# Optimization experiments

Hardware: AMD Instinct MI355X
Metric: run time of the kernel (lower is better)

Reference implementation:

```python
import jax, jax.numpy as jnp
import numpy as np

H = 8
D_MODEL = 1024
D_K = D_MODEL // H
NEG = -1000000000.0


def layer_norm(x, a, b, eps=1e-06):
    # torch std: unbiased (ddof=1); module divides by (std + eps)
    mean = jnp.mean(x, axis=-1, keepdims=True)
    var = jnp.sum((x - mean) ** 2, axis=-1, keepdims=True) / (x.shape[-1] - 1)
    std = jnp.sqrt(var)
    return a * (x - mean) / (std + eps) + b


def setup_inputs() -> dict:
    key = jax.random.key(0)
    ks = jax.random.split(key, 12)
    B, S, D = 8, 1024, D_MODEL
    inp = {
        "query": jax.random.normal(ks[0], (B, S, D), jnp.float32),
        "value": jax.random.normal(ks[1], (B, S, D), jnp.float32),
        "key": jax.random.normal(ks[2], (B, S, D), jnp.float32),
        "mask": jax.random.randint(ks[3], (B, S), 0, 2, jnp.int32),
        "ln_a": jnp.ones((D,), jnp.float32),
        "ln_b": jnp.zeros((D,), jnp.float32),
        "wq": jax.random.normal(ks[4], (D, D), jnp.float32) * 0.02,
        "bq": jnp.zeros((D,), jnp.float32),
        "wk": jax.random.normal(ks[5], (D, D), jnp.float32) * 0.02,
        "bk": jnp.zeros((D,), jnp.float32),
        "wv": jax.random.normal(ks[6], (D, D), jnp.float32) * 0.02,
        "bv": jnp.zeros((D,), jnp.float32),
        "w_aoa": jax.random.normal(ks[7], (2 * D, 2 * D), jnp.float32) * 0.02,  # [out, in]
        "b_aoa": jnp.zeros((2 * D,), jnp.float32),
    }
    return inp


def reference(query, value, key, mask, ln_a, ln_b, wq, bq, wk, bk, wv, bv, w_aoa, b_aoa):
    B, S, D = query.shape
    # mask [B,S] -> [B,1,1,S]
    m = mask[:, None, None, :]
    # norm_q
    q = layer_norm(query, ln_a, ln_b)
    # QKV projections, split heads -> [B,H,S,Dk]
    def split_heads(x):
        return x.reshape(B, -1, H, D_K).transpose(0, 2, 1, 3)
    q_ = split_heads(q @ wq.T + bq)
    k_ = split_heads(key @ wk.T + bk)
    v_ = split_heads(value @ wv.T + bv)
    scores = jnp.einsum("bhqd,bhkd->bhqk", q_, k_) / jnp.sqrt(jnp.float32(D_K))
    scores = jnp.where(m == 0, NEG, scores)
    p = jax.nn.softmax(scores, axis=-1)
    x = jnp.einsum("bhqk,bhkd->bhqd", p, v_)
    x = x.transpose(0, 2, 1, 3).reshape(B, S, D)
    # AoA: concat with (normed) query, linear to 2D, GLU
    z = jnp.concatenate([x, q], axis=-1) @ w_aoa.T + b_aoa
    a, g = jnp.split(z, 2, axis=-1)
    return a * jax.nn.sigmoid(g)
```

## Files before the change

kernel.cpp:

```cpp
#include <hip/hip_runtime.h>

typedef __attribute__((ext_vector_type(8))) __bf16 bf16x8;
typedef __attribute__((ext_vector_type(4))) float f32x4;
typedef __attribute__((ext_vector_type(16))) float f32x16;
typedef __attribute__((ext_vector_type(2))) int i32x2;

__device__ __forceinline__ ushort f2b(float f) {
    uint u = __builtin_bit_cast(uint, f);
    u += 0x7fffu + ((u >> 16) & 1u);
    return (ushort)(u >> 16);
}
__device__ __forceinline__ float b2f(ushort h) {
    uint u = ((uint)h) << 16;
    return __builtin_bit_cast(float, u);
}
__device__ __forceinline__ uint cvtpk(float a, float b) {
    uint r;
    asm("v_cvt_pk_bf16_f32 %0, %1, %2" : "=v"(r) : "v"(a), "v"(b));
    return r;
}

__global__ __launch_bounds__(256) void cast2_kernel(const float* __restrict__ s0,
                                                    const float* __restrict__ s1,
                                                    ushort* __restrict__ dst) {
    int bid = blockIdx.x;
    const float* src = (bid < 8192) ? s0 : s1;
    size_t so = ((size_t)(bid & 8191) * 256 + threadIdx.x) * 4;
    float4 v = *(const float4*)(src + so);
    ushort4 o;
    o.x = f2b(v.x); o.y = f2b(v.y); o.z = f2b(v.z); o.w = f2b(v.w);
    *(ushort4*)(dst + (size_t)bid * 1024 + threadIdx.x * 4) = o;
}

__global__ __launch_bounds__(256) void cast3_kernel(const float* __restrict__ s0,
                                                    const float* __restrict__ s1,
                                                    const float* __restrict__ s2,
                                                    ushort* __restrict__ dst) {
    int bid = blockIdx.x;
    const float* src = (bid < 1024) ? s0 : ((bid < 2048) ? s1 : s2);
    size_t so = ((size_t)(bid & 1023) * 256 + threadIdx.x) * 4;
    float4 v = *(const float4*)(src + so);
    ushort4 o;
    o.x = f2b(v.x); o.y = f2b(v.y); o.z = f2b(v.z); o.w = f2b(v.w);
    *(ushort4*)(dst + (size_t)bid * 1024 + threadIdx.x * 4) = o;
}

__global__ __launch_bounds__(256) void cast_permute_aoa(const float* __restrict__ src,
                                                        ushort* __restrict__ dst) {
    int n1 = blockIdx.x >> 1;
    int c = (blockIdx.x & 1) * 1024 + threadIdx.x * 4;
    int q = ((n1 & 63) | ((n1 >> 7) << 6)) + ((n1 >> 6) & 1) * 1024;
    float4 v = *(const float4*)(src + (size_t)q * 2048 + c);
    ushort4 o;
    o.x = f2b(v.x); o.y = f2b(v.y); o.z = f2b(v.z); o.w = f2b(v.w);
    *(ushort4*)(dst + (size_t)n1 * 2048 + c) = o;
}

__global__ __launch_bounds__(256) void ln_kernel(const float* __restrict__ x,
                                                 const float* __restrict__ ga,
                                                 const float* __restrict__ be,
                                                 ushort* __restrict__ xq) {
    const int row = blockIdx.x, tid = threadIdx.x;
    __shared__ float red[4];
    float4 v = ((const float4*)(x + (size_t)row * 1024))[tid];
    float sm = v.x + v.y + v.z + v.w;
    for (int off = 32; off; off >>= 1) sm += __shfl_xor(sm, off);
    if ((tid & 63) == 0) red[tid >> 6] = sm;
    __syncthreads();
    float mean = (red[0] + red[1] + red[2] + red[3]) * (1.f / 1024.f);
    __syncthreads();
    float dx = v.x - mean, dy = v.y - mean, dz = v.z - mean, dw = v.w - mean;
    float s2 = dx * dx + dy * dy + dz * dz + dw * dw;
    for (int off = 32; off; off >>= 1) s2 += __shfl_xor(s2, off);
    if ((tid & 63) == 0) red[tid >> 6] = s2;
    __syncthreads();
    float var = (red[0] + red[1] + red[2] + red[3]) * (1.f / 1023.f);
    float inv = 1.f / (sqrtf(var) + 1e-6f);
    float4 g = ((const float4*)ga)[tid];
    float4 bb = ((const float4*)be)[tid];
    ushort4 o;
    o.x = f2b(g.x * dx * inv + bb.x);
    o.y = f2b(g.y * dy * inv + bb.y);
    o.z = f2b(g.z * dz * inv + bb.z);
    o.w = f2b(g.w * dw * inv + bb.w);
    *(ushort4*)&xq[(size_t)row * 2048 + 1024 + tid * 4] = o;
}

template <int MODE>
__global__ __launch_bounds__(512, 2) void gemm6(const ushort* __restrict__ Aq, int ldaq,
                                                const ushort* __restrict__ B, int ldb,
                                                const float* __restrict__ bias0,
                                                void* __restrict__ out0,
                                                int K, int NB) {
    __shared__ ushort lds[2][32768];

    const int tid = threadIdx.x;
    const int w = tid >> 6, l = tid & 63;
    const int wr = w >> 2, wcn = w & 3;
    const int r16 = l & 15, g4 = l >> 4;

    const int bid = blockIdx.x;
    const int cpx = gridDim.x >> 3;
    const int swz = (bid & 7) * cpx + (bid >> 3);
    const int m0 = (swz / NB) * 256;
    const int n0 = (swz % NB) * 256;

    const ushort* A = Aq;
    const int lda = ldaq;

    const int srow8 = l >> 3;
    const int sxor8 = ((l & 7) ^ srow8) * 8;
    const ushort* As0 = A + (size_t)(m0 + w * 8 + srow8) * lda + sxor8;
    const ushort* Bs0 = B + (size_t)(n0 + w * 8 + srow8) * ldb + sxor8;

    f32x4 acc[8][4];
#pragma unroll
    for (int i = 0; i < 8; i++)
#pragma unroll
        for (int j = 0; j < 4; j++) acc[i][j] = (f32x4){0.f, 0.f, 0.f, 0.f};

    const int sw16 = (r16 & 7) << 4;
    char* ldsb = (char*)&lds[0][0];

#define STAGE_H(sel_, HS_, kt_)                                                            \
    do {                                                                                   \
        const int mat_ = (HS_)&1, half_ = (HS_) >> 1;                                      \
        const ushort* sb_ = mat_ ? Bs0 : As0;                                              \
        const int ld_ = mat_ ? ldb : lda;                                                  \
        _Pragma("unroll") for (int li_ = 0; li_ < 2; li_++) {                              \
            const ushort* src_ = sb_ + (size_t)(half_ * 128 + li_ * 64) * ld_ + (kt_)*64;  \
            int dst_ = (sel_)*65536 + mat_ * 32768 + half_ * 16384 + li_ * 8192 + w * 1024;\
            __builtin_amdgcn_global_load_lds(                                              \
                (const __attribute__((address_space(1))) void*)src_,                       \
                (__attribute__((address_space(3))) void*)(ldsb + dst_), 16, 0, 0);         \
        }                                                                                  \
    } while (0)

    auto LDA4 = [&](bf16x8 (&dst)[4][2], int sel, int half) {
#pragma unroll
        for (int ai = 0; ai < 4; ai++)
#pragma unroll
            for (int ks = 0; ks < 2; ks++)
                dst[ai][ks] = *(const bf16x8*)(ldsb + sel * 65536 + half * 16384 +
                                               (wr * 16 + 32 * ai + r16) * 128 +
                                               ((ks * 64 + g4 * 16) ^ sw16));
    };
    auto LDB2 = [&](bf16x8 (&dst)[2][2], int sel, int half) {
#pragma unroll
        for (int bi = 0; bi < 2; bi++)
#pragma unroll
            for (int ks = 0; ks < 2; ks++)
                dst[bi][ks] = *(const bf16x8*)(ldsb + sel * 65536 + 32768 + half * 16384 +
                                               (wcn * 16 + 64 * bi + r16) * 128 +
                                               ((ks * 64 + g4 * 16) ^ sw16));
    };
    auto MM = [&](bf16x8 (&af)[4][2], bf16x8 (&bf)[2][2], int A0, int B0) {
        __builtin_amdgcn_s_setprio(1);
#pragma unroll
        for (int ks = 0; ks < 2; ks++)
#pragma unroll
            for (int ai = 0; ai < 4; ai++)
#pragma unroll
                for (int bi = 0; bi < 2; bi++)
                    acc[A0 + ai][B0 + bi] = __builtin_amdgcn_mfma_f32_16x16x32_bf16(
                        af[ai][ks], bf[bi][ks], acc[A0 + ai][B0 + bi], 0, 0, 0);
        __builtin_amdgcn_s_setprio(0);
    };

    const int NT = K >> 6;

    STAGE_H(0, 0, 0); STAGE_H(0, 1, 0); STAGE_H(0, 2, 0); STAGE_H(0, 3, 0);
    STAGE_H(1, 0, 1); STAGE_H(1, 1, 1); STAGE_H(1, 2, 1);
    asm volatile("s_waitcnt vmcnt(10)" ::: "memory");
    __builtin_amdgcn_s_barrier();

    bf16x8 aL[4][2], aH[4][2], bL[2][2], bH[2][2];

    for (int t = 0; t < NT - 2; ++t) {
        const int sel = t & 1;
        LDA4(aL, sel, 0); LDB2(bL, sel, 0);
        STAGE_H(sel ^ 1, 3, t + 1);
        __builtin_amdgcn_s_barrier();
        MM(aL, bL, 0, 0);
        asm volatile("s_waitcnt vmcnt(10)" ::: "memory");
        __builtin_amdgcn_s_barrier();
        LDA4(aH, sel, 1);
        STAGE_H(sel, 0, t + 2);
        __builtin_amdgcn_s_barrier();
        MM(aH, bL, 4, 0);
        asm volatile("s_waitcnt vmcnt(10)" ::: "memory");
        __builtin_amdgcn_s_barrier();
        LDB2(bH, sel, 1);
        STAGE_H(sel, 1, t + 2);
        __builtin_amdgcn_s_barrier();
        MM(aH, bH, 4, 2);
        __builtin_amdgcn_s_barrier();
        STAGE_H(sel, 2, t + 2);
        __builtin_amdgcn_s_barrier();
        MM(aL, bH, 0, 2);
        asm volatile("s_waitcnt vmcnt(10)" ::: "memory");
        __builtin_amdgcn_s_barrier();
    }
    {
        const int sel = (NT - 2) & 1;
        LDA4(aL, sel, 0); LDB2(bL, sel, 0);
        STAGE_H(sel ^ 1, 3, NT - 1);
        __builtin_amdgcn_s_barrier();
        MM(aL, bL, 0, 0);
        asm volatile("s_waitcnt vmcnt(10)" ::: "memory");
        __builtin_amdgcn_s_barrier();
        LDA4(aH, sel, 1);
        __builtin_amdgcn_s_barrier();
        MM(aH, bL, 4, 0);
        asm volatile("s_waitcnt vmcnt(8)" ::: "memory");
        __builtin_amdgcn_s_barrier();
        LDB2(bH, sel, 1);
        __builtin_amdgcn_s_barrier();
        MM(aH, bH, 4, 2);
        __builtin_amdgcn_s_barrier();
        MM(aL, bH, 0, 2);
        asm volatile("s_waitcnt vmcnt(4)" ::: "memory");
        __builtin_amdgcn_s_barrier();
    }
    {
        const int sel = (NT - 1) & 1;
        LDA4(aL, sel, 0); LDB2(bL, sel, 0);
        __builtin_amdgcn_s_barrier();
        MM(aL, bL, 0, 0);
        asm volatile("s_waitcnt vmcnt(2)" ::: "memory");
        __builtin_amdgcn_s_barrier();
        LDA4(aH, sel, 1);
        __builtin_amdgcn_s_barrier();
        MM(aH, bL, 4, 0);
        asm volatile("s_waitcnt vmcnt(0)" ::: "memory");
        __builtin_amdgcn_s_barrier();
        LDB2(bH, sel, 1);
        MM(aH, bH, 4, 2);
        MM(aL, bH, 0, 2);
    }
#undef STAGE_H

    float* out = (float*)out0;
#pragma unroll
    for (int bp = 0; bp < 2; bp++) {
        int j = (n0 >> 1) + wcn * 16 + 64 * bp + r16;
        float bsa = bias0[j];
        float bsg = bias0[j + 1024];
#pragma unroll
        for (int a_ = 0; a_ < 8; a_++) {
            int mr = m0 + wr * 16 + 32 * a_ + g4 * 4;
#pragma unroll
            for (int r = 0; r < 4; r++) {
                float av = acc[a_][2 * bp][r] + bsa;
                float gv = acc[a_][2 * bp + 1][r] + bsg;
                out[(size_t)(mr + r) * 1024 + j] = av * (1.f / (1.f + __expf(-gv)));
            }
        }
    }
}

__global__ __launch_bounds__(512, 2) void gemm7(const ushort* __restrict__ Aq, int ldaq,
                                                const ushort* __restrict__ Ak,
                                                const ushort* __restrict__ Av,
                                                const ushort* __restrict__ B, int ldb,
                                                const float* __restrict__ bias0,
                                                const float* __restrict__ bias1,
                                                const float* __restrict__ bias2,
                                                ushort* __restrict__ out0,
                                                ushort* __restrict__ out1,
                                                ushort* __restrict__ out2,
                                                float qscale) {
    __shared__ ushort lds[2][24576];

    const int tid = threadIdx.x;
    const int w = tid >> 6, l = tid & 63;
    const int wr = w >> 2, wcn = w & 3;
    const int r16 = l & 15, g4 = l >> 4;

    const int bid = blockIdx.x;
    const int cpx = gridDim.x >> 3;
    const int swz = (bid & 7) * cpx + (bid >> 3);
    const int m0 = (swz / 12) * 128;
    const int n0 = (swz % 12) * 256;

    const int region = n0 >> 10;
    const ushort* A = region == 0 ? Aq : (region == 1 ? Ak : Av);
    const int lda = region == 0 ? ldaq : 1024;

    const int srow8 = l >> 3;
    const int sxor8 = ((l & 7) ^ srow8) * 8;
    const ushort* As0 = A + (size_t)(m0 + w * 8 + srow8) * lda + sxor8;
    const ushort* Bs0 = B + (size_t)(n0 + w * 8 + srow8) * ldb + sxor8;

    f32x4 acc[4][4];
#pragma unroll
    for (int i = 0; i < 4; i++)
#pragma unroll
        for (int j = 0; j < 4; j++) acc[i][j] = (f32x4){0.f, 0.f, 0.f, 0.f};

    const int sw16 = (r16 & 7) << 4;
    char* ldsb = (char*)&lds[0][0];

#define STAGE_A(sel_, h_, kt_)                                                             \
    __builtin_amdgcn_global_load_lds(                                                      \
        (const __attribute__((address_space(1))) void*)(As0 + (size_t)((h_)*64) * lda + (kt_)*64), \
        (__attribute__((address_space(3))) void*)(ldsb + (sel_)*49152 + (h_)*8192 + w * 1024), 16, 0, 0)
#define STAGE_B(sel_, h_, li_, kt_)                                                        \
    __builtin_amdgcn_global_load_lds(                                                      \
        (const __attribute__((address_space(1))) void*)(Bs0 + (size_t)((h_)*128 + (li_)*64) * ldb + (kt_)*64), \
        (__attribute__((address_space(3))) void*)(ldsb + (sel_)*49152 + 16384 + (h_)*16384 + (li_)*8192 + w * 1024), 16, 0, 0)

    auto LDA2 = [&](bf16x8 (&dst)[2][2], int sel, int half) {
#pragma unroll
        for (int ai = 0; ai < 2; ai++)
#pragma unroll
            for (int ks = 0; ks < 2; ks++)
                dst[ai][ks] = *(const bf16x8*)(ldsb + sel * 49152 + half * 8192 +
                                               (wr * 16 + 32 * ai + r16) * 128 +
                                               ((ks * 64 + g4 * 16) ^ sw16));
    };
    auto LDB2 = [&](bf16x8 (&dst)[2][2], int sel, int half) {
#pragma unroll
        for (int bi = 0; bi < 2; bi++)
#pragma unroll
            for (int ks = 0; ks < 2; ks++)
                dst[bi][ks] = *(const bf16x8*)(ldsb + sel * 49152 + 16384 + half * 16384 +
                                               (wcn * 16 + 64 * bi + r16) * 128 +
                                               ((ks * 64 + g4 * 16) ^ sw16));
    };
    auto MM = [&](bf16x8 (&af)[2][2], bf16x8 (&bf)[2][2], int A0, int B0) {
        __builtin_amdgcn_s_setprio(1);
#pragma unroll
        for (int ks = 0; ks < 2; ks++)
#pragma unroll
            for (int ai = 0; ai < 2; ai++)
#pragma unroll
                for (int bi = 0; bi < 2; bi++)
                    acc[A0 + ai][B0 + bi] = __builtin_amdgcn_mfma_f32_16x16x32_bf16(
                        af[ai][ks], bf[bi][ks], acc[A0 + ai][B0 + bi], 0, 0, 0);
        __builtin_amdgcn_s_setprio(0);
    };

    const int NT = 16;

    STAGE_A(0, 0, 0); STAGE_B(0, 0, 0, 0); STAGE_B(0, 0, 1, 0);
    STAGE_A(0, 1, 0); STAGE_B(0, 1, 0, 0); STAGE_B(0, 1, 1, 0);
    STAGE_A(1, 0, 1); STAGE_B(1, 0, 0, 1); STAGE_B(1, 0, 1, 1);
    STAGE_A(1, 1, 1);
    asm volatile("s_waitcnt vmcnt(7)" ::: "memory");
    __builtin_amdgcn_s_barrier();

    bf16x8 aL[2][2], aH[2][2], bL[2][2], bH[2][2];

    for (int t = 0; t < NT - 2; ++t) {
        const int sel = t & 1;
        LDA2(aL, sel, 0); LDB2(bL, sel, 0);
        STAGE_B(sel ^ 1, 1, 0, t + 1); STAGE_B(sel ^ 1, 1, 1, t + 1);
        __builtin_amdgcn_s_barrier();
        MM(aL, bL, 0, 0);
        asm volatile("s_waitcnt vmcnt(8)" ::: "memory");
        __builtin_amdgcn_s_barrier();
        LDA2(aH, sel, 1);
        STAGE_A(sel, 0, t + 2);
        __builtin_amdgcn_s_barrier();
        MM(aH, bL, 2, 0);
        asm volatile("s_waitcnt vmcnt(7)" ::: "memory");
        __builtin_amdgcn_s_barrier();
        LDB2(bH, sel, 1);
        STAGE_B(sel, 0, 0, t + 2); STAGE_B(sel, 0, 1, t + 2);
        __builtin_amdgcn_s_barrier();
        MM(aH, bH, 2, 2);
        __builtin_amdgcn_s_barrier();
        STAGE_A(sel, 1, t + 2);
        __builtin_amdgcn_s_barrier();
        MM(aL, bH, 0, 2);
        asm volatile("s_waitcnt vmcnt(7)" ::: "memory");
        __builtin_amdgcn_s_barrier();
    }
    {
        const int sel = (NT - 2) & 1;
        LDA2(aL, sel, 0); LDB2(bL, sel, 0);
        STAGE_B(sel ^ 1, 1, 0, NT - 1); STAGE_B(sel ^ 1, 1, 1, NT - 1);
        __builtin_amdgcn_s_barrier();
        MM(aL, bL, 0, 0);
        asm volatile("s_waitcnt vmcnt(8)" ::: "memory");
        __builtin_amdgcn_s_barrier();
        LDA2(aH, sel, 1);
        __builtin_amdgcn_s_barrier();
        MM(aH, bL, 2, 0);
        asm volatile("s_waitcnt vmcnt(6)" ::: "memory");
        __builtin_amdgcn_s_barrier();
        LDB2(bH, sel, 1);
        __builtin_amdgcn_s_barrier();
        MM(aH, bH, 2, 2);
        __builtin_amdgcn_s_barrier();
        MM(aL, bH, 0, 2);
        asm volatile("s_waitcnt vmcnt(3)" ::: "memory");
        __builtin_amdgcn_s_barrier();
    }
    {
        const int sel = (NT - 1) & 1;
        LDA2(aL, sel, 0); LDB2(bL, sel, 0);
        __builtin_amdgcn_s_barrier();
        MM(aL, bL, 0, 0);
        asm volatile("s_waitcnt vmcnt(2)" ::: "memory");
        __builtin_amdgcn_s_barrier();
        LDA2(aH, sel, 1);
        __builtin_amdgcn_s_barrier();
        MM(aH, bL, 2, 0);
        asm volatile("s_waitcnt vmcnt(0)" ::: "memory");
        __builtin_amdgcn_s_barrier();
        LDB2(bH, sel, 1);
        MM(aH, bH, 2, 2);
        MM(aL, bH, 0, 2);
    }
#undef STAGE_A
#undef STAGE_B

    const int nr0 = n0 & 1023;
    const float* bias = region == 0 ? bias0 : (region == 1 ? bias1 : bias2);
    const float scale = region == 0 ? qscale : 1.f;
    if (region < 2) {
        ushort* C = region == 0 ? out0 : out1;
#pragma unroll
        for (int b_ = 0; b_ < 4; b_++) {
            int n = nr0 + wcn * 16 + 64 * b_ + r16;
            float bs = bias[n];
#pragma unroll
            for (int a_ = 0; a_ < 4; a_++) {
                int mr = m0 + wr * 16 + 32 * a_ + g4 * 4;
#pragma unroll
                for (int r = 0; r < 4; r++)
                    C[(size_t)(mr + r) * 1024 + n] = f2b((acc[a_][b_][r] + bs) * scale);
            }
        }
    } else {
        ushort* Vt = out2;
#pragma unroll
        for (int b_ = 0; b_ < 4; b_++) {
            int n = nr0 + wcn * 16 + 64 * b_ + r16;
            float bs = bias[n];
            int h = n >> 7, d = n & 127;
#pragma unroll
            for (int a_ = 0; a_ < 4; a_++) {
                int mr = m0 + wr * 16 + 32 * a_ + g4 * 4;
                int bb = mr >> 10, s_ = mr & 1023;
                ushort4 o;
                o.x = f2b(acc[a_][b_][0] + bs);
                o.y = f2b(acc[a_][b_][1] + bs);
                o.z = f2b(acc[a_][b_][2] + bs);
                o.w = f2b(acc[a_][b_][3] + bs);
                *(ushort4*)&Vt[((size_t)(bb * 8 + h) * 128 + d) * 1024 + s_] = o;
            }
        }
    }
}

__global__ __launch_bounds__(256, 2) void attn_kernel(const ushort* __restrict__ Q,
                                                      const ushort* __restrict__ Kt,
                                                      const ushort* __restrict__ Vt,
                                                      const int* __restrict__ mask,
                                                      ushort* __restrict__ xq) {
    __shared__ ushort Ks[2][8192];
    __shared__ ushort Vs[2][8192];

    const int tid = threadIdx.x;
    const int l = tid & 63, wid = tid >> 6;
    const int ql = l & 31, hi = l >> 5;
    const int id = blockIdx.x;
    const int bh = ((id >> 6) << 3) | (id & 7);
    const int qb = (id >> 3) & 7;
    const int b = bh >> 3, h = bh & 7;
    const int q0 = qb * 128 + wid * 32;

    bf16x8 qf[8];
    const ushort* Qrow = Q + (size_t)(b * 1024 + q0 + ql) * 1024 + h * 128 + hi * 8;
#pragma unroll
    for (int ks = 0; ks < 8; ks++) qf[ks] = *(const bf16x8*)(Qrow + ks * 16);

    const ushort* Kg = Kt + ((size_t)b * 1024) * 1024 + h * 128;
    const ushort* Vg = Vt + (size_t)(b * 8 + h) * 128 * 1024;
    const int* mptr = mask + b * 1024;

    f32x16 xacc[4];
#pragma unroll
    for (int i = 0; i < 4; i++)
#pragma unroll
        for (int r = 0; r < 16; r++) xacc[i][r] = 0.f;
    float mrow = -INFINITY, lrow = 0.f, sclp = 0.f;
    bf16x8 pa[4];

    auto STAGE_K = [&](int sel, int t) {
        const int kv0 = t * 64;
#pragma unroll
        for (int it = 0; it < 4; ++it) {
            int ob = it * 4096 + wid * 1024;
            int o = ob + l * 16;
            int row = o >> 8;
            int sc = (o & 255) ^ ((row & 7) << 4);
            const ushort* src = Kg + (size_t)(kv0 + row) * 1024 + (sc >> 1);
            __builtin_amdgcn_global_load_lds((const __attribute__((address_space(1))) void*)src,
                (__attribute__((address_space(3))) void*)((char*)&Ks[sel][0] + ob), 16, 0, 0);
        }
    };
    auto STAGE_V = [&](int sel, int t) {
        const int kv0 = t * 64;
#pragma unroll
        for (int it = 0; it < 4; ++it) {
            int ob = it * 4096 + wid * 1024;
            int o = ob + l * 16;
            int d = o >> 7;
            int sc = (o & 127) ^ ((d & 7) << 4);
            const ushort* src = Vg + (size_t)d * 1024 + kv0 + (sc >> 1);
            __builtin_amdgcn_global_load_lds((const __attribute__((address_space(1))) void*)src,
                (__attribute__((address_space(3))) void*)((char*)&Vs[sel][0] + ob), 16, 0, 0);
        }
    };

    auto QK = [&](f32x16 (&s)[2], int sel, unsigned long long wt) {
        const char* Kb_ = (const char*)&Ks[sel][0];
#pragma unroll
        for (int sub = 0; sub < 2; sub++) {
            f32x16 sacc;
#pragma unroll
            for (int r = 0; r < 16; r++) sacc[r] = 0.f;
            const int rowk = sub * 32 + ql;
            const char* kr = Kb_ + rowk * 256;
            const int sw = (rowk & 7) << 4;
            __builtin_amdgcn_s_setprio(1);
#pragma unroll
            for (int ks = 0; ks < 8; ks++) {
                bf16x8 kfr = *(const bf16x8*)(kr + ((ks * 32 + hi * 16) ^ sw));
                sacc = __builtin_amdgcn_mfma_f32_32x32x16_bf16(kfr, qf[ks], sacc, 0, 0, 0);
            }
            __builtin_amdgcn_s_setprio(0);
#pragma unroll
            for (int q2 = 0; q2 < 4; q2++) {
                uint nib = (uint)(wt >> (8 * q2 + 4 * hi + 32 * sub)) & 15u;
#pragma unroll
                for (int r = 0; r < 4; r++)
                    if (!((nib >> r) & 1u)) sacc[4 * q2 + r] = -1e9f;
            }
            s[sub] = sacc;
        }
    };
    auto PV = [&](int sel) {
        const char* Vb_ = (const char*)&Vs[sel][0];
#pragma unroll
        for (int df = 0; df < 4; df++)
#pragma unroll
            for (int r = 0; r < 16; r++) xacc[df][r] *= sclp;
        __builtin_amdgcn_s_setprio(1);
#pragma unroll
        for (int ks2 = 0; ks2 < 4; ks2++) {
#pragma unroll
            for (int df = 0; df < 4; df++) {
                const int d = df * 32 + ql;
                bf16x8 vfr = *(const bf16x8*)(Vb_ + d * 128 + ((ks2 * 32 + hi * 16) ^ ((d & 7) << 4)));
                xacc[df] = __builtin_amdgcn_mfma_f32_32x32x16_bf16(vfr, pa[ks2], xacc[df], 0, 0, 0);
            }
        }
        __builtin_amdgcn_s_setprio(0);
    };
    auto SOFTMAX = [&](f32x16 (&s)[2]) {
        float pmax = -INFINITY;
#pragma unroll
        for (int res = 0; res < 2; res++)
#pragma unroll
            for (int r = 0; r < 16; r++) pmax = fmaxf(pmax, s[res][r]);
        pmax = fmaxf(pmax, __shfl_xor(pmax, 32));
        float mn = fmaxf(mrow, pmax);
        sclp = __expf(mrow - mn);
        mrow = mn;
        float rsum = 0.f;
#pragma unroll
        for (int res = 0; res < 2; res++)
#pragma unroll
            for (int r = 0; r < 16; r++) {
                float p = __expf(s[res][r] - mn);
                s[res][r] = p;
                rsum += p;
            }
        rsum += __shfl_xor(rsum, 32);
        lrow = lrow * sclp + rsum;
#pragma unroll
        for (int sub = 0; sub < 2; sub++)
#pragma unroll
            for (int g = 0; g < 2; g++) {
                const int b0 = g * 8;
                uint lo01 = cvtpk(s[sub][b0 + 0], s[sub][b0 + 1]);
                uint lo23 = cvtpk(s[sub][b0 + 2], s[sub][b0 + 3]);
                uint hi01 = cvtpk(s[sub][b0 + 4], s[sub][b0 + 5]);
                uint hi23 = cvtpk(s[sub][b0 + 6], s[sub][b0 + 7]);
                i32x2 r02 = __builtin_amdgcn_permlane32_swap((int)lo01, (int)hi01, false, false);
                i32x2 r13 = __builtin_amdgcn_permlane32_swap((int)lo23, (int)hi23, false, false);
                union { bf16x8 v; uint u[4]; } pk;
                pk.u[0] = (uint)r02.x;
                pk.u[1] = (uint)r13.x;
                pk.u[2] = (uint)r02.y;
                pk.u[3] = (uint)r13.y;
                pa[sub * 2 + g] = pk.v;
            }
    };

    STAGE_K(0, 0);
    int mv = mptr[l];
    asm volatile("s_waitcnt vmcnt(0)" ::: "memory");
    __syncthreads();
    STAGE_K(1, 1);
    STAGE_V(0, 0);
    unsigned long long wt = __ballot(mv != 0);
    mv = mptr[64 + l];
    f32x16 s[2];
    QK(s, 0, wt);
    SOFTMAX(s);
    int kc = 1, vc = 0;

    for (int u = 1; u < 16; ++u) {
        wt = __ballot(mv != 0);
        asm volatile("s_waitcnt vmcnt(0)" ::: "memory");
        __syncthreads();
        if (u < 15) STAGE_K(kc ^ 1, u + 1);
        STAGE_V(vc ^ 1, u);
        if (u < 15) mv = mptr[(u + 1) * 64 + l];

        QK(s, kc, wt);
        PV(vc);
        SOFTMAX(s);

        kc ^= 1; vc ^= 1;
    }

    asm volatile("s_waitcnt vmcnt(0)" ::: "memory");
    __syncthreads();
    PV(vc);

    const float inv = 1.f / lrow;
    const size_t orow = (size_t)(b * 1024 + q0 + ql) * 2048 + h * 128;
#pragma unroll
    for (int df = 0; df < 4; df++) {
#pragma unroll
        for (int q2 = 0; q2 < 4; q2++) {
            ushort4 o;
            o.x = f2b(xacc[df][4 * q2 + 0] * inv);
            o.y = f2b(xacc[df][4 * q2 + 1] * inv);
            o.z = f2b(xacc[df][4 * q2 + 2] * inv);
            o.w = f2b(xacc[df][4 * q2 + 3] * inv);
            *(ushort4*)&xq[orow + df * 32 + 8 * q2 + 4 * hi] = o;
        }
    }
}

extern "C" void kernel_launch(void* const* d_in, const int* in_sizes, int n_in,
                              void* d_out, int out_size, void* d_ws, size_t ws_size,
                              hipStream_t stream) {
    const float* query = (const float*)d_in[0];
    const float* value = (const float*)d_in[1];
    const float* key   = (const float*)d_in[2];
    const int*   mask  = (const int*)d_in[3];
    const float* ln_a  = (const float*)d_in[4];
    const float* ln_b  = (const float*)d_in[5];
    const float* wq    = (const float*)d_in[6];
    const float* bq    = (const float*)d_in[7];
    const float* wk    = (const float*)d_in[8];
    const float* bk    = (const float*)d_in[9];
    const float* wv    = (const float*)d_in[10];
    const float* bv    = (const float*)d_in[11];
    const float* waoa  = (const float*)d_in[12];
    const float* baoa  = (const float*)d_in[13];
    float* out = (float*)d_out;

    char* w8 = (char*)d_ws;
    ushort* xq   = (ushort*)(w8);
    ushort* Qb   = (ushort*)(w8 + 33554432);
    ushort* Kb   = (ushort*)(w8 + 50331648);
    ushort* Vt   = (ushort*)(w8 + 67108864);
    ushort* keyb = (ushort*)(w8 + 83886080);
    ushort* wqb  = (ushort*)(w8 + 117440512);
    ushort* wab  = (ushort*)(w8 + 123731968);

    cast2_kernel<<<16384, 256, 0, stream>>>(key, value, keyb);
    cast3_kernel<<<3072, 256, 0, stream>>>(wq, wk, wv, wqb);
    cast_permute_aoa<<<4096, 256, 0, stream>>>(waoa, wab);
    ln_kernel<<<8192, 256, 0, stream>>>(query, ln_a, ln_b, xq);

    const float qscale = 0.08838834764831845f;
    ushort* valb = keyb + 8388608;

    gemm7<<<768, 512, 0, stream>>>(xq + 1024, 2048, keyb, valb,
                                   wqb, 1024, bq, bk, bv,
                                   Qb, Kb, Vt, qscale);

    attn_kernel<<<512, 256, 0, stream>>>(Qb, Kb, Vt, mask, xq);

    gemm6<1><<<256, 512, 0, stream>>>(xq, 2048, wab, 2048, baoa, out, 2048, 8);
}
```

Baseline: 228.0 us.

## Merge cast kernels and add lazy softmax rescaling with split QK accumulators

Folds the three fp32-to-bf16 cast kernels into one launch, which removes two kernel launches and their tail gaps. In attention, the QK dot product now uses two independent MFMA accumulator chains to shorten the dependency chain. The per-row max uses a tree reduction. The online-softmax rescale of the output accumulator is skipped whenever the new max exceeds the running max by at most 8 for every lane in the wavefront. This lazy rescaling adds a wave-wide vote and lets exp values grow up to e^8 before renormalisation, which costs some numerical headroom in the bf16 probabilities.

```diff
diff --git a/kernel.cpp b/kernel.cpp
--- a/kernel.cpp
+++ b/kernel.cpp
@@ -20,40 +20,40 @@
     return r;
 }
 
-__global__ __launch_bounds__(256) void cast2_kernel(const float* __restrict__ s0,
-                                                    const float* __restrict__ s1,
-                                                    ushort* __restrict__ dst) {
+__global__ __launch_bounds__(256) void cast_all(const float* __restrict__ key,
+                                                const float* __restrict__ value,
+                                                const float* __restrict__ wq,
+                                                const float* __restrict__ wk,
+                                                const float* __restrict__ wv,
+                                                const float* __restrict__ waoa,
+                                                ushort* __restrict__ keyb,
+                                                ushort* __restrict__ wqb,
+                                                ushort* __restrict__ wab) {
     int bid = blockIdx.x;
-    const float* src = (bid < 8192) ? s0 : s1;
-    size_t so = ((size_t)(bid & 8191) * 256 + threadIdx.x) * 4;
-    float4 v = *(const float4*)(src + so);
-    ushort4 o;
-    o.x = f2b(v.x); o.y = f2b(v.y); o.z = f2b(v.z); o.w = f2b(v.w);
-    *(ushort4*)(dst + (size_t)bid * 1024 + threadIdx.x * 4) = o;
-}
-
-__global__ __launch_bounds__(256) void cast3_kernel(const float* __restrict__ s0,
-                                                    const float* __restrict__ s1,
-                                                    const float* __restrict__ s2,
-                                                    ushort* __restrict__ dst) {
-    int bid = blockIdx.x;
-    const float* src = (bid < 1024) ? s0 : ((bid < 2048) ? s1 : s2);
-    size_t so = ((size_t)(bid & 1023) * 256 + threadIdx.x) * 4;
-    float4 v = *(const float4*)(src + so);
-    ushort4 o;
-    o.x = f2b(v.x); o.y = f2b(v.y); o.z = f2b(v.z); o.w = f2b(v.w);
-    *(ushort4*)(dst + (size_t)bid * 1024 + threadIdx.x * 4) = o;
-}
-
-__global__ __launch_bounds__(256) void cast_permute_aoa(const float* __restrict__ src,
-                                                        ushort* __restrict__ dst) {
-    int n1 = blockIdx.x >> 1;
-    int c = (blockIdx.x & 1) * 1024 + threadIdx.x * 4;
-    int q = ((n1 & 63) | ((n1 >> 7) << 6)) + ((n1 >> 6) & 1) * 1024;
-    float4 v = *(const float4*)(src + (size_t)q * 2048 + c);
-    ushort4 o;
-    o.x = f2b(v.x); o.y = f2b(v.y); o.z = f2b(v.z); o.w = f2b(v.w);
-    *(ushort4*)(dst + (size_t)n1 * 2048 + c) = o;
+    int tid = threadIdx.x;
+    if (bid < 16384) {
+        const float* src = (bid < 8192) ? key : value;
+        float4 v = *(const float4*)(src + ((size_t)(bid & 8191) * 256 + tid) * 4);
+        ushort4 o;
+        o.x = f2b(v.x); o.y = f2b(v.y); o.z = f2b(v.z); o.w = f2b(v.w);
+        *(ushort4*)(keyb + (size_t)bid * 1024 + tid * 4) = o;
+    } else if (bid < 19456) {
+        int b2 = bid - 16384;
+        const float* src = (b2 < 1024) ? wq : ((b2 < 2048) ? wk : wv);
+        float4 v = *(const float4*)(src + ((size_t)(b2 & 1023) * 256 + tid) * 4);
+        ushort4 o;
+        o.x = f2b(v.x); o.y = f2b(v.y); o.z = f2b(v.z); o.w = f2b(v.w);
+        *(ushort4*)(wqb + (size_t)b2 * 1024 + tid * 4) = o;
+    } else {
+        int b3 = bid - 19456;
+        int n1 = b3 >> 1;
+        int c = (b3 & 1) * 1024 + tid * 4;
+        int q = ((n1 & 63) | ((n1 >> 7) << 6)) + ((n1 >> 6) & 1) * 1024;
+        float4 v = *(const float4*)(waoa + (size_t)q * 2048 + c);
+        ushort4 o;
+        o.x = f2b(v.x); o.y = f2b(v.y); o.z = f2b(v.z); o.w = f2b(v.w);
+        *(ushort4*)(wab + (size_t)n1 * 2048 + c) = o;
+    }
 }
 
 __global__ __launch_bounds__(256) void ln_kernel(const float* __restrict__ x,
@@ -488,6 +488,7 @@
 #pragma unroll
         for (int r = 0; r < 16; r++) xacc[i][r] = 0.f;
     float mrow = -INFINITY, lrow = 0.f, sclp = 0.f;
+    bool resc = true;
     bf16x8 pa[4];
 
     auto STAGE_K = [&](int sel, int t) {
@@ -521,35 +522,41 @@
         const char* Kb_ = (const char*)&Ks[sel][0];
 #pragma unroll
         for (int sub = 0; sub < 2; sub++) {
-            f32x16 sacc;
-#pragma unroll
-            for (int r = 0; r < 16; r++) sacc[r] = 0.f;
+            f32x16 sa, sb;
+#pragma unroll
+            for (int r = 0; r < 16; r++) { sa[r] = 0.f; sb[r] = 0.f; }
             const int rowk = sub * 32 + ql;
             const char* kr = Kb_ + rowk * 256;
             const int sw = (rowk & 7) << 4;
             __builtin_amdgcn_s_setprio(1);
 #pragma unroll
-            for (int ks = 0; ks < 8; ks++) {
-                bf16x8 kfr = *(const bf16x8*)(kr + ((ks * 32 + hi * 16) ^ sw));
-                sacc = __builtin_amdgcn_mfma_f32_32x32x16_bf16(kfr, qf[ks], sacc, 0, 0, 0);
+            for (int ks = 0; ks < 4; ks++) {
+                bf16x8 k0 = *(const bf16x8*)(kr + (((2 * ks) * 32 + hi * 16) ^ sw));
+                bf16x8 k1 = *(const bf16x8*)(kr + (((2 * ks + 1) * 32 + hi * 16) ^ sw));
+                sa = __builtin_amdgcn_mfma_f32_32x32x16_bf16(k0, qf[2 * ks], sa, 0, 0, 0);
+                sb = __builtin_amdgcn_mfma_f32_32x32x16_bf16(k1, qf[2 * ks + 1], sb, 0, 0, 0);
             }
             __builtin_amdgcn_s_setprio(0);
 #pragma unroll
+            for (int r = 0; r < 16; r++) sa[r] += sb[r];
+#pragma unroll
             for (int q2 = 0; q2 < 4; q2++) {
                 uint nib = (uint)(wt >> (8 * q2 + 4 * hi + 32 * sub)) & 15u;
 #pragma unroll
                 for (int r = 0; r < 4; r++)
-                    if (!((nib >> r) & 1u)) sacc[4 * q2 + r] = -1e9f;
+                    if (!((nib >> r) & 1u)) sa[4 * q2 + r] = -1e9f;
             }
-            s[sub] = sacc;
+            s[sub] = sa;
         }
     };
     auto PV = [&](int sel) {
         const char* Vb_ = (const char*)&Vs[sel][0];
-#pragma unroll
-        for (int df = 0; df < 4; df++)
-#pragma unroll
-            for (int r = 0; r < 16; r++) xacc[df][r] *= sclp;
+        if (resc) {
+#pragma unroll
+            for (int df = 0; df < 4; df++)
+#pragma unroll
+                for (int r = 0; r < 16; r++) xacc[df][r] *= sclp;
+        }
         __builtin_amdgcn_s_setprio(1);
 #pragma unroll
         for (int ks2 = 0; ks2 < 4; ks2++) {
@@ -563,26 +570,34 @@
         __builtin_amdgcn_s_setprio(0);
     };
     auto SOFTMAX = [&](f32x16 (&s)[2]) {
-        float pmax = -INFINITY;
+        float v[16];
+#pragma unroll
+        for (int r = 0; r < 16; r++) v[r] = fmaxf(s[0][r], s[1][r]);
+#pragma unroll
+        for (int st = 8; st; st >>= 1)
+#pragma unroll
+            for (int i = 0; i < 8; i++)
+                if (i < st) v[i] = fmaxf(v[i], v[i + st]);
+        float pmax = fmaxf(v[0], __shfl_xor(v[0], 32));
+        if (!__all(pmax - mrow <= 8.f)) {
+            float mn = fmaxf(mrow, pmax);
+            sclp = __expf(mrow - mn);
+            mrow = mn;
+            resc = true;
+        } else {
+            resc = false;
+        }
+        float rsum = 0.f;
 #pragma unroll
         for (int res = 0; res < 2; res++)
 #pragma unroll
-            for (int r = 0; r < 16; r++) pmax = fmaxf(pmax, s[res][r]);
-        pmax = fmaxf(pmax, __shfl_xor(pmax, 32));
-        float mn = fmaxf(mrow, pmax);
-        sclp = __expf(mrow - mn);
-        mrow = mn;
-        float rsum = 0.f;
-#pragma unroll
-        for (int res = 0; res < 2; res++)
-#pragma unroll
             for (int r = 0; r < 16; r++) {
-                float p = __expf(s[res][r] - mn);
+                float p = __expf(s[res][r] - mrow);
                 s[res][r] = p;
                 rsum += p;
             }
         rsum += __shfl_xor(rsum, 32);
-        lrow = lrow * sclp + rsum;
+        lrow = (resc ? lrow * sclp : lrow) + rsum;
 #pragma unroll
         for (int sub = 0; sub < 2; sub++)
 #pragma unroll
@@ -594,12 +609,12 @@
                 uint hi23 = cvtpk(s[sub][b0 + 6], s[sub][b0 + 7]);
                 i32x2 r02 = __builtin_amdgcn_permlane32_swap((int)lo01, (int)hi01, false, false);
                 i32x2 r13 = __builtin_amdgcn_permlane32_swap((int)lo23, (int)hi23, false, false);
-                union { bf16x8 v; uint u[4]; } pk;
+                union { bf16x8 vv; uint u[4]; } pk;
                 pk.u[0] = (uint)r02.x;
                 pk.u[1] = (uint)r13.x;
                 pk.u[2] = (uint)r02.y;
                 pk.u[3] = (uint)r13.y;
-                pa[sub * 2 + g] = pk.v;
+                pa[sub * 2 + g] = pk.vv;
             }
     };
 
@@ -679,9 +694,7 @@
     ushort* wqb  = (ushort*)(w8 + 117440512);
     ushort* wab  = (ushort*)(w8 + 123731968);
 
-    cast2_kernel<<<16384, 256, 0, stream>>>(key, value, keyb);
-    cast3_kernel<<<3072, 256, 0, stream>>>(wq, wk, wv, wqb);
-    cast_permute_aoa<<<4096, 256, 0, stream>>>(waoa, wab);
+    cast_all<<<23552, 256, 0, stream>>>(key, value, wq, wk, wv, waoa, keyb, wqb, wab);
     ln_kernel<<<8192, 256, 0, stream>>>(query, ln_a, ln_b, xq);
 
     const float qscale = 0.08838834764831845f;
```

After: 229.1 us. No clear change (+0.5%).
